# Optimization experiments

Measured on AMD Instinct MI355X. Metric: run time of the kernel, lower is better.

The kernel has to match this reference:

```python
import jax, jax.numpy as jnp
import numpy as np

B, L, D, H, NLAYERS = 32, 2048, 1024, 16, 4
HD = D // H
NEG = -1e30


def setup_inputs() -> dict:
    key = jax.random.key(0)
    ks = jax.random.split(key, 12)
    tokens = jax.random.normal(ks[0], (B, L, D), dtype=jnp.float32)
    lengths = jax.random.randint(ks[1], (B,), 1, L + 1, dtype=jnp.int32)
    query_token = jax.random.normal(ks[2], (1, D), dtype=jnp.float32)
    s = 0.02
    Wq = jax.random.normal(ks[3], (NLAYERS, D, D), dtype=jnp.float32) * s
    Wk = jax.random.normal(ks[4], (NLAYERS, D, D), dtype=jnp.float32) * s
    Wv = jax.random.normal(ks[5], (NLAYERS, D, D), dtype=jnp.float32) * s
    Wo = jax.random.normal(ks[6], (NLAYERS, D, D), dtype=jnp.float32) * s
    bq = jnp.zeros((NLAYERS, D), jnp.float32)
    bk = jnp.zeros((NLAYERS, D), jnp.float32)
    bv = jnp.zeros((NLAYERS, D), jnp.float32)
    bo = jnp.zeros((NLAYERS, D), jnp.float32)
    gamma = jnp.ones((NLAYERS, D), jnp.float32)
    beta = jnp.zeros((NLAYERS, D), jnp.float32)
    return dict(tokens=tokens, lengths=lengths, query_token=query_token,
                Wq=Wq, bq=bq, Wk=Wk, bk=bk, Wv=Wv, bv=bv, Wo=Wo, bo=bo,
                gamma=gamma, beta=beta)


def _layernorm(x, g, b):
    mu = jnp.mean(x, axis=-1, keepdims=True)
    var = jnp.mean(jnp.square(x - mu), axis=-1, keepdims=True)
    return (x - mu) * jax.lax.rsqrt(var + 1e-5) * g + b


def reference(tokens, lengths, query_token, Wq, bq, Wk, bk, Wv, bv, Wo, bo, gamma, beta):
    # valid[b, l] = True where token l exists (inverse of key_padding_mask)
    valid = jnp.arange(L)[None, :] < lengths[:, None]            # [B, L]
    scale = 1.0 / jnp.sqrt(jnp.float32(HD))
    # zero out padded positions like the torch padded buffer (math-neutral)
    toks = tokens * valid[:, :, None].astype(tokens.dtype)       # [B, L, D]
    q = jnp.broadcast_to(query_token[None], (B, 1, D))           # [B, 1, D]
    for i in range(NLAYERS):
        qh = (q @ Wq[i] + bq[i]).reshape(B, 1, H, HD)            # [B, 1, H, hd]
        kh = (toks @ Wk[i] + bk[i]).reshape(B, L, H, HD)         # [B, L, H, hd]
        vh = (toks @ Wv[i] + bv[i]).reshape(B, L, H, HD)
        scores = jnp.einsum('bqhd,bkhd->bhqk', qh, kh) * scale   # [B, H, 1, L]
        scores = jnp.where(valid[:, None, None, :], scores, NEG)
        attn = jax.nn.softmax(scores, axis=-1)
        out = jnp.einsum('bhqk,bkhd->bqhd', attn, vh).reshape(B, 1, D)
        out = out @ Wo[i] + bo[i]
        q = _layernorm(out, gamma[i], beta[i])
    return q[:, 0, :]                                            # [B, D]
```

## Files before the change

kernel.cpp:

```cpp
#include <hip/hip_runtime.h>
#include <hip/hip_bf16.h>
#include <cstdint>
#include <cstddef>

#define BB 32
#define LL 2048
#define DD 1024
#define HH 16
#define HDIM 64
#define NL 4
#define NCHUNK 8
#define CHUNK 256
#define NEGINF -1e30f
#define PKS 16

typedef __attribute__((ext_vector_type(8))) short bf16x8;
typedef __attribute__((ext_vector_type(4))) float f32x4;

__device__ __forceinline__ unsigned short f2b(float x) {
    union { float f; unsigned int u; } v; v.f = x;
    unsigned int r = (v.u + 0x7FFFu + ((v.u >> 16) & 1u)) >> 16;
    return (unsigned short)r;
}
__device__ __forceinline__ float b2f(unsigned short u) {
    union { unsigned int u; float f; } v; v.u = ((unsigned int)u) << 16;
    return v.f;
}

template<int SRC>
__global__ __launch_bounds__(256) void k_gemv(
        const float* __restrict__ Xg,
        const float* __restrict__ stats, const float* __restrict__ gamma,
        const float* __restrict__ beta,
        const float* __restrict__ parts_in, const float* __restrict__ bias_in,
        const unsigned short* __restrict__ ctx16, const float* __restrict__ m_p,
        const float* __restrict__ s_p,
        const float* __restrict__ W, float* __restrict__ outp) {
    constexpr int KL = DD / PKS;
    int bid = blockIdx.x, tid = threadIdx.x;
    int ct = bid & 15, ks = bid >> 4;
    int e0 = ks * KL;
    __shared__ float Xs[BB][KL];
    __shared__ float wgtS[BB][NCHUNK];
    __shared__ float mgS[BB], SgS[BB];
    if (SRC == 3) {
        if (tid < BB) {
            int b = tid; float m = NEGINF;
            for (int c8 = 0; c8 < NCHUNK; ++c8)
                m = fmaxf(m, m_p[(b * NCHUNK + c8) * HH + ct]);
            float S = 0.f;
            for (int c8 = 0; c8 < NCHUNK; ++c8)
                S += s_p[(b * NCHUNK + c8) * HH + ct] *
                     __expf(m_p[(b * NCHUNK + c8) * HH + ct] - m);
            mgS[b] = m; SgS[b] = S;
        }
        __syncthreads();
        {
            int b = tid >> 3, c8 = tid & 7;
            wgtS[b][c8] = __expf(m_p[(b * NCHUNK + c8) * HH + ct] - mgS[b]) / SgS[b];
        }
        __syncthreads();
    }
#pragma unroll
    for (int j = 0; j < 8; ++j) {
        int i = tid + j * 256;
        int b = i >> 6, k = i & 63;
        float x;
        if (SRC == 0) {
            x = Xg[e0 + k];
        } else if (SRC == 1) {
            float mu = stats[b * 2], rstd = stats[b * 2 + 1];
            x = (Xg[(size_t)b * DD + e0 + k] - mu) * rstd * gamma[e0 + k] + beta[e0 + k];
        } else if (SRC == 2) {
            x = bias_in[e0 + k];
#pragma unroll
            for (int j2 = 0; j2 < PKS; ++j2)
                x += parts_in[((size_t)(j2 * BB) + b) * DD + e0 + k];
        } else {
            x = 0.f;
#pragma unroll
            for (int c8 = 0; c8 < NCHUNK; ++c8)
                x += wgtS[b][c8] *
                     b2f(ctx16[(((size_t)(b * NCHUNK + c8)) * HH + ct) * DD + e0 + k]);
        }
        Xs[b][k] = x;
    }
    __syncthreads();
    int col = tid & 63, bg = tid >> 6;
    int c = ct * 64 + col;
    float acc[8] = {0.f, 0.f, 0.f, 0.f, 0.f, 0.f, 0.f, 0.f};
    for (int k = 0; k < KL; k += 4) {
        float w0 = W[(size_t)(e0 + k) * DD + c];
        float w1 = W[(size_t)(e0 + k + 1) * DD + c];
        float w2 = W[(size_t)(e0 + k + 2) * DD + c];
        float w3 = W[(size_t)(e0 + k + 3) * DD + c];
#pragma unroll
        for (int bb = 0; bb < 8; ++bb) {
            const float4 xv = *(const float4*)&Xs[bg * 8 + bb][k];
            acc[bb] += xv.x * w0 + xv.y * w1 + xv.z * w2 + xv.w * w3;
        }
    }
#pragma unroll
    for (int bb = 0; bb < 8; ++bb)
        outp[((size_t)(ks * BB) + bg * 8 + bb) * DD + c] = acc[bb];
}

template<int LAST>
__global__ __launch_bounds__(1024) void k_stats(const float* __restrict__ parts,
        const float* __restrict__ bo, const float* __restrict__ gamma,
        const float* __restrict__ beta, float* __restrict__ oraw,
        float* __restrict__ stats, float* __restrict__ outp) {
    int b = blockIdx.x, c = threadIdx.x;
    float v = bo[c];
#pragma unroll
    for (int ks = 0; ks < PKS; ++ks)
        v += parts[((size_t)(ks * BB) + b) * DD + c];
    if (!LAST) oraw[(size_t)b * DD + c] = v;
    float s1 = v, s2 = v * v;
#pragma unroll
    for (int off = 32; off; off >>= 1) {
        s1 += __shfl_xor(s1, off);
        s2 += __shfl_xor(s2, off);
    }
    __shared__ float r1[16], r2[16];
    __shared__ float smu, srs;
    int w = c >> 6;
    if ((c & 63) == 0) { r1[w] = s1; r2[w] = s2; }
    __syncthreads();
    if (c == 0) {
        float a = 0.f, q = 0.f;
#pragma unroll
        for (int i = 0; i < 16; ++i) { a += r1[i]; q += r2[i]; }
        float mu = a / (float)DD, var = q / (float)DD - mu * mu;
        float rs = rsqrtf(var + 1e-5f);
        smu = mu; srs = rs;
        stats[b * 2] = mu;
        stats[b * 2 + 1] = rs;
    }
    __syncthreads();
    if (LAST)
        outp[(size_t)b * DD + c] = (v - smu) * srs * gamma[c] + beta[c];
}

__global__ __launch_bounds__(256) void k_wk(const float* __restrict__ qp,
        const float* __restrict__ bq,
        const float* __restrict__ Wk, const float* __restrict__ bk,
        unsigned short* __restrict__ wk16, float* __restrict__ sb) {
    int h = blockIdx.x >> 4, et = blockIdx.x & 15;
    int tid = threadIdx.x;
    __shared__ float qs[BB][HDIM + 1];
    for (int i = tid; i < BB * HDIM; i += 256) {
        int bb = i >> 6, d = i & 63;
        float v = bq[h * HDIM + d];
#pragma unroll
        for (int ks = 0; ks < PKS; ++ks)
            v += qp[((size_t)(ks * BB + bb)) * DD + h * HDIM + d];
        qs[bb][d] = v;
    }
    __syncthreads();
    int b = tid & 31, eo = tid >> 5;
    for (int k = 0; k < 8; ++k) {
        int e = et * 64 + eo * 8 + k;
        const float* wrow = Wk + (size_t)e * DD + h * HDIM;
        float acc = 0.f;
#pragma unroll
        for (int d = 0; d < HDIM; ++d) acc += qs[b][d] * wrow[d];
        wk16[((size_t)(b * HH + h)) * DD + e] = f2b(acc);
    }
    if (et == 0 && tid < BB) {
        float acc = 0.f;
#pragma unroll
        for (int d = 0; d < HDIM; ++d) acc += qs[tid][d] * bk[h * HDIM + d];
        sb[tid * HH + h] = acc;
    }
}

template<int MODE>
__global__ __launch_bounds__(1024) void k_attn(const float* __restrict__ toks,
        unsigned short* __restrict__ tcache,
        const int* __restrict__ lens, const unsigned short* __restrict__ wk16,
        const float* __restrict__ sb, unsigned short* __restrict__ ctx16,
        float* __restrict__ m_p, float* __restrict__ s_p) {
    int b = blockIdx.x >> 3, chunk = blockIdx.x & 7;
    int tid = threadIdx.x, lane = tid & 63, w = tid >> 6;
    int len = lens[b];
    int base = chunk * CHUNK;
    int pidx = (b * NCHUNK + chunk) * HH;
    if (base >= len) {
        if (tid < HH) { m_p[pidx + tid] = NEGINF; s_p[pidx + tid] = 0.f; }
        return;
    }
    int nv = min(CHUNK, len - base);

    __shared__ __align__(16) unsigned short Tr[32][1032];
    __shared__ float Sred[16][HH][34];
    __shared__ unsigned short Pt[HH][40];
    __shared__ float sm_m[HH], sm_s[HH], sm_c[HH];

    if (tid < HH) { sm_m[tid] = NEGINF; sm_s[tid] = 0.f; }

    int hq = lane & 15, qg = lane >> 4;
    const unsigned short* wkb = wk16 + ((size_t)(b * HH + hq)) * DD + w * 64 + 8 * qg;
    bf16x8 afr0 = *(const bf16x8*)(wkb);
    bf16x8 afr1 = *(const bf16x8*)(wkb + 32);
    f32x4 zer = {0.f, 0.f, 0.f, 0.f};
    f32x4 ctxacc[4] = {zer, zer, zer, zer};
    float sbh = (tid < 512) ? sb[b * HH + (tid >> 5)] : 0.f;
    int st = tid >> 7;
    int se = (tid & 127) * 8;
    __syncthreads();

    for (int g = 0; g < 8; ++g) {
        int t0 = g * 32;
        if (t0 >= nv) break;
        if (MODE == 2) {
            const unsigned short* srcr = tcache + ((size_t)(b * LL + base + t0)) * DD;
#pragma unroll
            for (int p = 0; p < 4; ++p) {
                int t = p * 8 + st;
                bf16x8 v = *(const bf16x8*)(srcr + (size_t)t * DD + se);
                *(bf16x8*)&Tr[t][se] = v;
            }
        } else {
            const float* srcr = toks + ((size_t)(b * LL + base + t0)) * DD;
#pragma unroll
            for (int p = 0; p < 4; ++p) {
                int t = p * 8 + st;
                const float* sp = srcr + (size_t)t * DD + se;
                float4 a0 = *(const float4*)sp;
                float4 a1 = *(const float4*)(sp + 4);
                bf16x8 v;
                v[0] = f2b(a0.x); v[1] = f2b(a0.y); v[2] = f2b(a0.z); v[3] = f2b(a0.w);
                v[4] = f2b(a1.x); v[5] = f2b(a1.y); v[6] = f2b(a1.z); v[7] = f2b(a1.w);
                *(bf16x8*)&Tr[t][se] = v;
                if (MODE == 1)
                    *(bf16x8*)(tcache + ((size_t)(b * LL + base + t0 + t)) * DD + se) = v;
            }
        }
        __syncthreads();
        f32x4 s0 = zer, s1 = zer;
        {
            int eb = w * 64 + 8 * qg;
            s0 = __builtin_amdgcn_mfma_f32_16x16x32_bf16(afr0, *(const bf16x8*)&Tr[hq][eb], s0, 0, 0, 0);
            s0 = __builtin_amdgcn_mfma_f32_16x16x32_bf16(afr1, *(const bf16x8*)&Tr[hq][eb + 32], s0, 0, 0, 0);
            s1 = __builtin_amdgcn_mfma_f32_16x16x32_bf16(afr0, *(const bf16x8*)&Tr[16 + hq][eb], s1, 0, 0, 0);
            s1 = __builtin_amdgcn_mfma_f32_16x16x32_bf16(afr1, *(const bf16x8*)&Tr[16 + hq][eb + 32], s1, 0, 0, 0);
        }
#pragma unroll
        for (int r = 0; r < 4; ++r) {
            Sred[w][qg * 4 + r][hq] = s0[r];
            Sred[w][qg * 4 + r][16 + hq] = s1[r];
        }
        __syncthreads();
        if (tid < 512) {
            int h = tid >> 5, t = tid & 31;
            float s = 0.f;
#pragma unroll
            for (int ww = 0; ww < 16; ++ww) s += Sred[ww][h][t];
            s = (s + sbh) * 0.125f;
            bool valid = (t0 + t) < nv;
            if (!valid) s = NEGINF;
            float tm = s;
#pragma unroll
            for (int off = 16; off; off >>= 1) tm = fmaxf(tm, __shfl_xor(tm, off, 32));
            float oldm = sm_m[h];
            float newm = fmaxf(oldm, tm);
            float pv = valid ? __expf(s - newm) : 0.f;
            float ps = pv;
#pragma unroll
            for (int off = 16; off; off >>= 1) ps += __shfl_xor(ps, off, 32);
            if (t == 0) {
                float corr = __expf(oldm - newm);
                sm_c[h] = corr;
                sm_m[h] = newm;
                sm_s[h] = sm_s[h] * corr + ps;
            }
            Pt[h][t] = f2b(pv);
        }
        __syncthreads();
        {
            float cr[4];
#pragma unroll
            for (int r = 0; r < 4; ++r) cr[r] = sm_c[qg * 4 + r];
            bf16x8 pafr;
            ushort4 pa0 = *(const ushort4*)&Pt[hq][8 * qg];
            ushort4 pa1 = *(const ushort4*)&Pt[hq][8 * qg + 4];
            pafr[0] = pa0.x; pafr[1] = pa0.y; pafr[2] = pa0.z; pafr[3] = pa0.w;
            pafr[4] = pa1.x; pafr[5] = pa1.y; pafr[6] = pa1.z; pafr[7] = pa1.w;
#pragma unroll
            for (int et = 0; et < 4; ++et) {
#pragma unroll
                for (int r = 0; r < 4; ++r) ctxacc[et][r] *= cr[r];
                bf16x8 bfr;
                int ec = w * 64 + et * 16 + hq;
#pragma unroll
                for (int i = 0; i < 8; ++i) bfr[i] = (short)Tr[8 * qg + i][ec];
                ctxacc[et] = __builtin_amdgcn_mfma_f32_16x16x32_bf16(pafr, bfr, ctxacc[et], 0, 0, 0);
            }
        }
        __syncthreads();
    }
    if (tid < HH) { m_p[pidx + tid] = sm_m[tid]; s_p[pidx + tid] = sm_s[tid]; }
#pragma unroll
    for (int et = 0; et < 4; ++et)
#pragma unroll
        for (int r = 0; r < 4; ++r) {
            int h = qg * 4 + r, e = w * 64 + et * 16 + hq;
            ctx16[((size_t)pidx + h) * DD + e] = f2b(ctxacc[et][r]);
        }
}

extern "C" void kernel_launch(void* const* d_in, const int* in_sizes, int n_in,
                              void* d_out, int out_size, void* d_ws, size_t ws_size,
                              hipStream_t stream) {
    const float* toks  = (const float*)d_in[0];
    const int*   lens  = (const int*)d_in[1];
    const float* qt    = (const float*)d_in[2];
    const float* Wq    = (const float*)d_in[3];
    const float* bq    = (const float*)d_in[4];
    const float* Wk    = (const float*)d_in[5];
    const float* bk    = (const float*)d_in[6];
    const float* Wv    = (const float*)d_in[7];
    const float* bv    = (const float*)d_in[8];
    const float* Wo    = (const float*)d_in[9];
    const float* bo    = (const float*)d_in[10];
    const float* gamma = (const float*)d_in[11];
    const float* beta  = (const float*)d_in[12];
    float* out = (float*)d_out;
    float* ws  = (float*)d_ws;

    unsigned short* ctx16 = (unsigned short*)ws;
    float* m_p   = ws + 2097152;
    float* s_p   = ws + 2101248;
    float* pvp   = ws + 2105344;
    float* op    = ws + 2629632;
    float* qp    = ws + 3153920;
    float* oraw  = ws + 3678208;
    float* stats = ws + 3710976;
    float* sbuf  = ws + 3711040;
    unsigned short* wk16 = (unsigned short*)(ws + 3711552);
    const size_t base_floats = 3973696;
    unsigned short* tcache = (unsigned short*)(ws + base_floats);
    const size_t need_cache = base_floats * 4 + (size_t)BB * LL * DD * 2;
    const bool use_cache = (ws_size >= need_cache);

    k_gemv<0><<<256, 256, 0, stream>>>(qt, nullptr, nullptr, nullptr,
            nullptr, nullptr, nullptr, nullptr, nullptr, Wq, qp);
    k_wk<<<256, 256, 0, stream>>>(qp, bq, Wk, bk, wk16, sbuf);

    for (int i = 0; i < NL; ++i) {
        if (use_cache) {
            if (i == 0)
                k_attn<1><<<256, 1024, 0, stream>>>(toks, tcache, lens, wk16,
                        sbuf, ctx16, m_p, s_p);
            else
                k_attn<2><<<256, 1024, 0, stream>>>(toks, tcache, lens, wk16,
                        sbuf, ctx16, m_p, s_p);
        } else {
            k_attn<0><<<256, 1024, 0, stream>>>(toks, tcache, lens, wk16,
                    sbuf, ctx16, m_p, s_p);
        }
        const float* Wv_i = Wv + (size_t)i * DD * DD;
        const float* Wo_i = Wo + (size_t)i * DD * DD;
        k_gemv<3><<<256, 256, 0, stream>>>(nullptr, nullptr, nullptr, nullptr,
                nullptr, nullptr, ctx16, m_p, s_p, Wv_i, pvp);
        k_gemv<2><<<256, 256, 0, stream>>>(nullptr, nullptr, nullptr, nullptr,
                pvp, bv + i * DD, nullptr, nullptr, nullptr, Wo_i, op);
        if (i == NL - 1) {
            k_stats<1><<<32, 1024, 0, stream>>>(op, bo + i * DD, gamma + i * DD,
                    beta + i * DD, oraw, stats, out);
        } else {
            k_stats<0><<<32, 1024, 0, stream>>>(op, bo + i * DD, gamma + i * DD,
                    beta + i * DD, oraw, stats, out);
            k_gemv<1><<<256, 256, 0, stream>>>(oraw, stats, gamma + i * DD,
                    beta + i * DD, nullptr, nullptr, nullptr, nullptr, nullptr,
                    Wq + (size_t)(i + 1) * DD * DD, qp);
            k_wk<<<256, 256, 0, stream>>>(qp, bq + (i + 1) * DD,
                    Wk + (size_t)(i + 1) * DD * DD, bk + (i + 1) * DD,
                    wk16, sbuf);
        }
    }
}
```

Baseline: 353.9 us.

## Halve attention chunk size to double blocks and fuse LayerNorm into Q projection

Measured after the change: 453.9 us. 1.28x slower.

```diff
diff --git a/kernel.cpp b/kernel.cpp
--- a/kernel.cpp
+++ b/kernel.cpp
@@ -9,8 +9,9 @@
 #define HH 16
 #define HDIM 64
 #define NL 4
-#define NCHUNK 8
-#define CHUNK 256
+#define NCHUNK 16
+#define CHUNK 128
+#define TBLK 16
 #define NEGINF -1e30f
 #define PKS 16
 
@@ -29,9 +30,6 @@
 
 template<int SRC>
 __global__ __launch_bounds__(256) void k_gemv(
-        const float* __restrict__ Xg,
-        const float* __restrict__ stats, const float* __restrict__ gamma,
-        const float* __restrict__ beta,
         const float* __restrict__ parts_in, const float* __restrict__ bias_in,
         const unsigned short* __restrict__ ctx16, const float* __restrict__ m_p,
         const float* __restrict__ s_p,
@@ -55,8 +53,10 @@
             mgS[b] = m; SgS[b] = S;
         }
         __syncthreads();
-        {
-            int b = tid >> 3, c8 = tid & 7;
+#pragma unroll
+        for (int j = 0; j < 2; ++j) {
+            int idx = tid + j * 256;
+            int b = idx >> 4, c8 = idx & 15;
             wgtS[b][c8] = __expf(m_p[(b * NCHUNK + c8) * HH + ct] - mgS[b]) / SgS[b];
         }
         __syncthreads();
@@ -66,12 +66,7 @@
         int i = tid + j * 256;
         int b = i >> 6, k = i & 63;
         float x;
-        if (SRC == 0) {
-            x = Xg[e0 + k];
-        } else if (SRC == 1) {
-            float mu = stats[b * 2], rstd = stats[b * 2 + 1];
-            x = (Xg[(size_t)b * DD + e0 + k] - mu) * rstd * gamma[e0 + k] + beta[e0 + k];
-        } else if (SRC == 2) {
+        if (SRC == 2) {
             x = bias_in[e0 + k];
 #pragma unroll
             for (int j2 = 0; j2 < PKS; ++j2)
@@ -105,17 +100,14 @@
         outp[((size_t)(ks * BB) + bg * 8 + bb) * DD + c] = acc[bb];
 }
 
-template<int LAST>
-__global__ __launch_bounds__(1024) void k_stats(const float* __restrict__ parts,
+__global__ __launch_bounds__(1024) void k_statsF(const float* __restrict__ parts,
         const float* __restrict__ bo, const float* __restrict__ gamma,
-        const float* __restrict__ beta, float* __restrict__ oraw,
-        float* __restrict__ stats, float* __restrict__ outp) {
+        const float* __restrict__ beta, float* __restrict__ outp) {
     int b = blockIdx.x, c = threadIdx.x;
     float v = bo[c];
 #pragma unroll
     for (int ks = 0; ks < PKS; ++ks)
         v += parts[((size_t)(ks * BB) + b) * DD + c];
-    if (!LAST) oraw[(size_t)b * DD + c] = v;
     float s1 = v, s2 = v * v;
 #pragma unroll
     for (int off = 32; off; off >>= 1) {
@@ -132,18 +124,106 @@
 #pragma unroll
         for (int i = 0; i < 16; ++i) { a += r1[i]; q += r2[i]; }
         float mu = a / (float)DD, var = q / (float)DD - mu * mu;
-        float rs = rsqrtf(var + 1e-5f);
-        smu = mu; srs = rs;
-        stats[b * 2] = mu;
-        stats[b * 2 + 1] = rs;
-    }
-    __syncthreads();
-    if (LAST)
-        outp[(size_t)b * DD + c] = (v - smu) * srs * gamma[c] + beta[c];
-}
-
-__global__ __launch_bounds__(256) void k_wk(const float* __restrict__ qp,
-        const float* __restrict__ bq,
+        smu = mu; srs = rsqrtf(var + 1e-5f);
+    }
+    __syncthreads();
+    outp[(size_t)b * DD + c] = (v - smu) * srs * gamma[c] + beta[c];
+}
+
+__global__ __launch_bounds__(256) void k_qnext(const float* __restrict__ op,
+        const float* __restrict__ bo, const float* __restrict__ gamma,
+        const float* __restrict__ beta, const float* __restrict__ Wq,
+        const float* __restrict__ bq, float* __restrict__ qh) {
+    int bid = blockIdx.x, tid = threadIdx.x;
+    int ct = bid & 15, bp = bid >> 4;
+    int b0 = bp * 2;
+    __shared__ float Xr[2][DD];
+    __shared__ float pr[4][2][64];
+    __shared__ float r1[4], r2[4];
+    __shared__ float smu[2], srs[2];
+#pragma unroll
+    for (int j = 0; j < 8; ++j) {
+        int idx = tid + j * 256;
+        int bb = idx >> 10, c = idx & (DD - 1);
+        float v = bo[c];
+#pragma unroll
+        for (int ks = 0; ks < PKS; ++ks)
+            v += op[((size_t)(ks * BB) + b0 + bb) * DD + c];
+        Xr[bb][c] = v;
+    }
+    __syncthreads();
+    {
+        int bb = tid >> 7, l = tid & 127;
+        float s1 = 0.f, s2 = 0.f;
+#pragma unroll
+        for (int j = 0; j < 8; ++j) {
+            float x = Xr[bb][l * 8 + j];
+            s1 += x; s2 += x * x;
+        }
+#pragma unroll
+        for (int off = 32; off; off >>= 1) {
+            s1 += __shfl_xor(s1, off);
+            s2 += __shfl_xor(s2, off);
+        }
+        int w = tid >> 6;
+        if ((tid & 63) == 0) { r1[w] = s1; r2[w] = s2; }
+    }
+    __syncthreads();
+    if (tid < 2) {
+        float a = r1[tid * 2] + r1[tid * 2 + 1];
+        float q = r2[tid * 2] + r2[tid * 2 + 1];
+        float mu = a / (float)DD, var = q / (float)DD - mu * mu;
+        smu[tid] = mu; srs[tid] = rsqrtf(var + 1e-5f);
+    }
+    __syncthreads();
+    {
+        int c = tid & 63, ks4 = tid >> 6;
+        float mu0 = smu[0], rs0 = srs[0], mu1 = smu[1], rs1 = srs[1];
+        float acc0 = 0.f, acc1 = 0.f;
+        int k0 = ks4 * 256;
+        for (int k = k0; k < k0 + 256; ++k) {
+            float g = gamma[k], be = beta[k];
+            float w = Wq[(size_t)k * DD + ct * 64 + c];
+            float x0 = (Xr[0][k] - mu0) * rs0 * g + be;
+            float x1 = (Xr[1][k] - mu1) * rs1 * g + be;
+            acc0 += x0 * w;
+            acc1 += x1 * w;
+        }
+        pr[ks4][0][c] = acc0;
+        pr[ks4][1][c] = acc1;
+    }
+    __syncthreads();
+    if (tid < 128) {
+        int bb = tid >> 6, c = tid & 63;
+        float q = bq[ct * 64 + c];
+#pragma unroll
+        for (int j = 0; j < 4; ++j) q += pr[j][bb][c];
+        qh[((size_t)(b0 + bb)) * DD + ct * 64 + c] = q;
+    }
+}
+
+__global__ __launch_bounds__(256) void k_q0(const float* __restrict__ qt,
+        const float* __restrict__ Wq, const float* __restrict__ bq,
+        float* __restrict__ qh) {
+    int ct = blockIdx.x, tid = threadIdx.x;
+    __shared__ float pr[4][64];
+    int c = tid & 63, ks4 = tid >> 6;
+    float acc = 0.f;
+    int k0 = ks4 * 256;
+    for (int k = k0; k < k0 + 256; ++k)
+        acc += qt[k] * Wq[(size_t)k * DD + ct * 64 + c];
+    pr[ks4][c] = acc;
+    __syncthreads();
+    if (tid < 64) {
+        float q = bq[ct * 64 + tid];
+#pragma unroll
+        for (int j = 0; j < 4; ++j) q += pr[j][tid];
+        qh[ct * 64 + tid] = q;
+    }
+}
+
+template<int BCAST>
+__global__ __launch_bounds__(256) void k_wk(const float* __restrict__ qh,
         const float* __restrict__ Wk, const float* __restrict__ bk,
         unsigned short* __restrict__ wk16, float* __restrict__ sb) {
     int h = blockIdx.x >> 4, et = blockIdx.x & 15;
@@ -151,11 +231,7 @@
     __shared__ float qs[BB][HDIM + 1];
     for (int i = tid; i < BB * HDIM; i += 256) {
         int bb = i >> 6, d = i & 63;
-        float v = bq[h * HDIM + d];
-#pragma unroll
-        for (int ks = 0; ks < PKS; ++ks)
-            v += qp[((size_t)(ks * BB + bb)) * DD + h * HDIM + d];
-        qs[bb][d] = v;
+        qs[bb][d] = qh[((size_t)(BCAST ? 0 : bb)) * DD + h * HDIM + d];
     }
     __syncthreads();
     int b = tid & 31, eo = tid >> 5;
@@ -181,7 +257,7 @@
         const int* __restrict__ lens, const unsigned short* __restrict__ wk16,
         const float* __restrict__ sb, unsigned short* __restrict__ ctx16,
         float* __restrict__ m_p, float* __restrict__ s_p) {
-    int b = blockIdx.x >> 3, chunk = blockIdx.x & 7;
+    int b = blockIdx.x >> 4, chunk = blockIdx.x & 15;
     int tid = threadIdx.x, lane = tid & 63, w = tid >> 6;
     int len = lens[b];
     int base = chunk * CHUNK;
@@ -192,12 +268,13 @@
     }
     int nv = min(CHUNK, len - base);
 
-    __shared__ __align__(16) unsigned short Tr[32][1032];
-    __shared__ float Sred[16][HH][34];
+    __shared__ __align__(16) unsigned short Tr[TBLK][1032];
+    __shared__ float Sred[16][HH][18];
     __shared__ unsigned short Pt[HH][40];
     __shared__ float sm_m[HH], sm_s[HH], sm_c[HH];
 
     if (tid < HH) { sm_m[tid] = NEGINF; sm_s[tid] = 0.f; }
+    if (tid < 256) Pt[tid >> 4][16 + (tid & 15)] = 0;
 
     int hq = lane & 15, qg = lane >> 4;
     const unsigned short* wkb = wk16 + ((size_t)(b * HH + hq)) * DD + w * 64 + 8 * qg;
@@ -205,55 +282,53 @@
     bf16x8 afr1 = *(const bf16x8*)(wkb + 32);
     f32x4 zer = {0.f, 0.f, 0.f, 0.f};
     f32x4 ctxacc[4] = {zer, zer, zer, zer};
-    float sbh = (tid < 512) ? sb[b * HH + (tid >> 5)] : 0.f;
-    int st = tid >> 7;
-    int se = (tid & 127) * 8;
-    __syncthreads();
-
-    for (int g = 0; g < 8; ++g) {
-        int t0 = g * 32;
+    float sbh = (tid < 256) ? sb[b * HH + (tid >> 4)] : 0.f;
+    int st = tid >> 6;
+    int se = (tid & 63) * 16;
+    const size_t rowbase = (size_t)(b * LL + base);
+    __syncthreads();
+
+    for (int g = 0; g < CHUNK / TBLK; ++g) {
+        int t0 = g * TBLK;
         if (t0 >= nv) break;
         if (MODE == 2) {
-            const unsigned short* srcr = tcache + ((size_t)(b * LL + base + t0)) * DD;
-#pragma unroll
-            for (int p = 0; p < 4; ++p) {
-                int t = p * 8 + st;
-                bf16x8 v = *(const bf16x8*)(srcr + (size_t)t * DD + se);
-                *(bf16x8*)&Tr[t][se] = v;
+            const unsigned short* sp = tcache + (rowbase + t0 + st) * DD + se;
+            bf16x8 v0 = *(const bf16x8*)sp;
+            bf16x8 v1 = *(const bf16x8*)(sp + 8);
+            *(bf16x8*)&Tr[st][se] = v0;
+            *(bf16x8*)&Tr[st][se + 8] = v1;
+        } else {
+            const float* sp = toks + (rowbase + t0 + st) * DD + se;
+            float4 a0 = *(const float4*)sp;
+            float4 a1 = *(const float4*)(sp + 4);
+            float4 a2 = *(const float4*)(sp + 8);
+            float4 a3 = *(const float4*)(sp + 12);
+            bf16x8 v0, v1;
+            v0[0] = f2b(a0.x); v0[1] = f2b(a0.y); v0[2] = f2b(a0.z); v0[3] = f2b(a0.w);
+            v0[4] = f2b(a1.x); v0[5] = f2b(a1.y); v0[6] = f2b(a1.z); v0[7] = f2b(a1.w);
+            v1[0] = f2b(a2.x); v1[1] = f2b(a2.y); v1[2] = f2b(a2.z); v1[3] = f2b(a2.w);
+            v1[4] = f2b(a3.x); v1[5] = f2b(a3.y); v1[6] = f2b(a3.z); v1[7] = f2b(a3.w);
+            *(bf16x8*)&Tr[st][se] = v0;
+            *(bf16x8*)&Tr[st][se + 8] = v1;
+            if (MODE == 1) {
+                unsigned short* cp = tcache + (rowbase + t0 + st) * DD + se;
+                *(bf16x8*)cp = v0;
+                *(bf16x8*)(cp + 8) = v1;
             }
-        } else {
-            const float* srcr = toks + ((size_t)(b * LL + base + t0)) * DD;
-#pragma unroll
-            for (int p = 0; p < 4; ++p) {
-                int t = p * 8 + st;
-                const float* sp = srcr + (size_t)t * DD + se;
-                float4 a0 = *(const float4*)sp;
-                float4 a1 = *(const float4*)(sp + 4);
-                bf16x8 v;
-                v[0] = f2b(a0.x); v[1] = f2b(a0.y); v[2] = f2b(a0.z); v[3] = f2b(a0.w);
-                v[4] = f2b(a1.x); v[5] = f2b(a1.y); v[6] = f2b(a1.z); v[7] = f2b(a1.w);
-                *(bf16x8*)&Tr[t][se] = v;
-                if (MODE == 1)
-                    *(bf16x8*)(tcache + ((size_t)(b * LL + base + t0 + t)) * DD + se) = v;
-            }
-        }
-        __syncthreads();
-        f32x4 s0 = zer, s1 = zer;
+        }
+        __syncthreads();
+        f32x4 s0 = zer;
         {
             int eb = w * 64 + 8 * qg;
             s0 = __builtin_amdgcn_mfma_f32_16x16x32_bf16(afr0, *(const bf16x8*)&Tr[hq][eb], s0, 0, 0, 0);
             s0 = __builtin_amdgcn_mfma_f32_16x16x32_bf16(afr1, *(const bf16x8*)&Tr[hq][eb + 32], s0, 0, 0, 0);
-            s1 = __builtin_amdgcn_mfma_f32_16x16x32_bf16(afr0, *(const bf16x8*)&Tr[16 + hq][eb], s1, 0, 0, 0);
-            s1 = __builtin_amdgcn_mfma_f32_16x16x32_bf16(afr1, *(const bf16x8*)&Tr[16 + hq][eb + 32], s1, 0, 0, 0);
-        }
-#pragma unroll
-        for (int r = 0; r < 4; ++r) {
+        }
+#pragma unroll
+        for (int r = 0; r < 4; ++r)
             Sred[w][qg * 4 + r][hq] = s0[r];
-            Sred[w][qg * 4 + r][16 + hq] = s1[r];
-        }
-        __syncthreads();
-        if (tid < 512) {
-            int h = tid >> 5, t = tid & 31;
+        __syncthreads();
+        if (tid < 256) {
+            int h = tid >> 4, t = tid & 15;
             float s = 0.f;
 #pragma unroll
             for (int ww = 0; ww < 16; ++ww) s += Sred[ww][h][t];
@@ -262,13 +337,13 @@
             if (!valid) s = NEGINF;
             float tm = s;
 #pragma unroll
-            for (int off = 16; off; off >>= 1) tm = fmaxf(tm, __shfl_xor(tm, off, 32));
+            for (int off = 8; off; off >>= 1) tm = fmaxf(tm, __shfl_xor(tm, off, 16));
             float oldm = sm_m[h];
             float newm = fmaxf(oldm, tm);
             float pv = valid ? __expf(s - newm) : 0.f;
             float ps = pv;
 #pragma unroll
-            for (int off = 16; off; off >>= 1) ps += __shfl_xor(ps, off, 32);
+            for (int off = 8; off; off >>= 1) ps += __shfl_xor(ps, off, 16);
             if (t == 0) {
                 float corr = __expf(oldm - newm);
                 sm_c[h] = corr;
@@ -294,7 +369,7 @@
                 bf16x8 bfr;
                 int ec = w * 64 + et * 16 + hq;
 #pragma unroll
-                for (int i = 0; i < 8; ++i) bfr[i] = (short)Tr[8 * qg + i][ec];
+                for (int i = 0; i < 8; ++i) bfr[i] = (short)Tr[(8 * qg + i) & 15][ec];
                 ctxacc[et] = __builtin_amdgcn_mfma_f32_16x16x32_bf16(pafr, bfr, ctxacc[et], 0, 0, 0);
             }
         }
@@ -330,54 +405,48 @@
     float* ws  = (float*)d_ws;
 
     unsigned short* ctx16 = (unsigned short*)ws;
-    float* m_p   = ws + 2097152;
-    float* s_p   = ws + 2101248;
-    float* pvp   = ws + 2105344;
-    float* op    = ws + 2629632;
-    float* qp    = ws + 3153920;
-    float* oraw  = ws + 3678208;
-    float* stats = ws + 3710976;
-    float* sbuf  = ws + 3711040;
-    unsigned short* wk16 = (unsigned short*)(ws + 3711552);
-    const size_t base_floats = 3973696;
+    float* m_p   = ws + 4194304;
+    float* s_p   = ws + 4202496;
+    float* pvp   = ws + 4210688;
+    float* op    = ws + 4734976;
+    float* qh    = ws + 5259264;
+    float* sbuf  = ws + 5292032;
+    unsigned short* wk16 = (unsigned short*)(ws + 5292544);
+    const size_t base_floats = 5554688;
     unsigned short* tcache = (unsigned short*)(ws + base_floats);
     const size_t need_cache = base_floats * 4 + (size_t)BB * LL * DD * 2;
     const bool use_cache = (ws_size >= need_cache);
 
-    k_gemv<0><<<256, 256, 0, stream>>>(qt, nullptr, nullptr, nullptr,
-            nullptr, nullptr, nullptr, nullptr, nullptr, Wq, qp);
-    k_wk<<<256, 256, 0, stream>>>(qp, bq, Wk, bk, wk16, sbuf);
+    k_q0<<<16, 256, 0, stream>>>(qt, Wq, bq, qh);
+    k_wk<1><<<256, 256, 0, stream>>>(qh, Wk, bk, wk16, sbuf);
 
     for (int i = 0; i < NL; ++i) {
         if (use_cache) {
             if (i == 0)
-                k_attn<1><<<256, 1024, 0, stream>>>(toks, tcache, lens, wk16,
+                k_attn<1><<<512, 1024, 0, stream>>>(toks, tcache, lens, wk16,
                         sbuf, ctx16, m_p, s_p);
             else
-                k_attn<2><<<256, 1024, 0, stream>>>(toks, tcache, lens, wk16,
+                k_attn<2><<<512, 1024, 0, stream>>>(toks, tcache, lens, wk16,
                         sbuf, ctx16, m_p, s_p);
         } else {
-            k_attn<0><<<256, 1024, 0, stream>>>(toks, tcache, lens, wk16,
+            k_attn<0><<<512, 1024, 0, stream>>>(toks, tcache, lens, wk16,
                     sbuf, ctx16, m_p, s_p);
         }
         const float* Wv_i = Wv + (size_t)i * DD * DD;
         const float* Wo_i = Wo + (size_t)i * DD * DD;
-        k_gemv<3><<<256, 256, 0, stream>>>(nullptr, nullptr, nullptr, nullptr,
-                nullptr, nullptr, ctx16, m_p, s_p, Wv_i, pvp);
-        k_gemv<2><<<256, 256, 0, stream>>>(nullptr, nullptr, nullptr, nullptr,
-                pvp, bv + i * DD, nullptr, nullptr, nullptr, Wo_i, op);
+        k_gemv<3><<<256, 256, 0, stream>>>(nullptr, nullptr, ctx16, m_p, s_p,
+                Wv_i, pvp);
+        k_gemv<2><<<256, 256, 0, stream>>>(pvp, bv + i * DD, nullptr, nullptr,
+                nullptr, Wo_i, op);
         if (i == NL - 1) {
-            k_stats<1><<<32, 1024, 0, stream>>>(op, bo + i * DD, gamma + i * DD,
-                    beta + i * DD, oraw, stats, out);
+            k_statsF<<<32, 1024, 0, stream>>>(op, bo + i * DD, gamma + i * DD,
+                    beta + i * DD, out);
         } else {
-            k_stats<0><<<32, 1024, 0, stream>>>(op, bo + i * DD, gamma + i * DD,
-                    beta + i * DD, oraw, stats, out);
-            k_gemv<1><<<256, 256, 0, stream>>>(oraw, stats, gamma + i * DD,
-                    beta + i * DD, nullptr, nullptr, nullptr, nullptr, nullptr,
-                    Wq + (size_t)(i + 1) * DD * DD, qp);
-            k_wk<<<256, 256, 0, stream>>>(qp, bq + (i + 1) * DD,
-                    Wk + (size_t)(i + 1) * DD * DD, bk + (i + 1) * DD,
-                    wk16, sbuf);
-        }
-    }
-}
+            k_qnext<<<256, 256, 0, stream>>>(op, bo + i * DD, gamma + i * DD,
+                    beta + i * DD, Wq + (size_t)(i + 1) * DD * DD,
+                    bq + (i + 1) * DD, qh);
+            k_wk<0><<<256, 256, 0, stream>>>(qh, Wk + (size_t)(i + 1) * DD * DD,
+                    bk + (i + 1) * DD, wk16, sbuf);
+        }
+    }
+}
```
